# Kernel tuning notes

Hardware: AMD Instinct MI355X
Metric: run time of the kernel (lower is better)

Reference implementation:

```python
import jax, jax.numpy as jnp
import numpy as np

WINDOW = 512
N_GLOBAL = 32


def setup_inputs() -> dict:
    key = jax.random.key(0)
    kq, kk, kv = jax.random.split(key, 3)
    shape = (2, 16, 8192, 64)  # [batch, heads, seq_len, head_dim]
    q = jax.random.normal(kq, shape, dtype=jnp.float32)
    k = jax.random.normal(kk, shape, dtype=jnp.float32)
    v = jax.random.normal(kv, shape, dtype=jnp.float32)
    return {"q": q, "k": k, "v": v}


def _sliding_window_attention(q, k, v):
    # Faithful to the torch loop: for i in range(0, S, W) the window is
    # [max(0, i-W//2), min(S, i+W//2)). For S a multiple of W these windows are
    # contiguous, non-overlapping chunks: chunk0 = [0, W//2), then (n-1) chunks
    # of width W. Concatenated output covers positions [0, S - W//2).
    B, H, S, D = q.shape
    W, G, half = WINDOW, N_GLOBAL, WINDOW // 2
    n = S // W
    scale = 1.0 / (D ** 0.5)

    kg = k[:, :, :G]  # [B,H,G,D] global keys
    vg = v[:, :, :G]

    # --- first chunk: positions [0, half) ---
    q0 = q[:, :, :half]
    kc0 = jnp.concatenate([kg, k[:, :, :half]], axis=2)  # [B,H,G+half,D]
    vc0 = jnp.concatenate([vg, v[:, :, :half]], axis=2)
    s0 = jnp.einsum('bhqd,bhkd->bhqk', q0, kc0) * scale
    o0 = jnp.einsum('bhqk,bhkd->bhqd', jax.nn.softmax(s0, axis=-1), vc0)

    # --- remaining (n-1) chunks of width W: positions [half, S-half) ---
    C = n - 1
    qr = q[:, :, half:S - half].reshape(B, H, C, W, D)
    kr = k[:, :, half:S - half].reshape(B, H, C, W, D)
    vr = v[:, :, half:S - half].reshape(B, H, C, W, D)
    kgb = jnp.broadcast_to(kg[:, :, None], (B, H, C, G, D))
    vgb = jnp.broadcast_to(vg[:, :, None], (B, H, C, G, D))
    kc = jnp.concatenate([kgb, kr], axis=3)  # [B,H,C,G+W,D]
    vc = jnp.concatenate([vgb, vr], axis=3)
    s = jnp.einsum('bhcqd,bhckd->bhcqk', qr, kc) * scale
    o = jnp.einsum('bhcqk,bhckd->bhcqd', jax.nn.softmax(s, axis=-1), vc)
    o = o.reshape(B, H, C * W, D)

    return jnp.concatenate([o0, o], axis=2)  # [B,H,S - W//2,D]


def reference(q, k, v):
    return _sliding_window_attention(q, k, v)
```

## Files before the change

kernel.cpp:

```cpp
#include <hip/hip_runtime.h>
#include <hip/hip_bf16.h>

typedef __bf16 v8bf16 __attribute__((ext_vector_type(8)));
typedef __bf16 v2bf16 __attribute__((ext_vector_type(2)));
typedef float  v4f    __attribute__((ext_vector_type(4)));
typedef float  v16f   __attribute__((ext_vector_type(16)));
typedef unsigned int u32;

#define SEQ     8192
#define DIM     64
#define OUTSEQ  7936
#define WIN     512
#define HALF    256
#define BH      32
#define NCHUNK  15
#define MAXT    17
#define NWG_CH  1920
#define VROWT   40

__device__ __forceinline__ v8bf16 cvt8(v4f a, v4f b) {
    v8bf16 r;
    r[0] = (__bf16)a[0]; r[1] = (__bf16)a[1];
    r[2] = (__bf16)a[2]; r[3] = (__bf16)a[3];
    r[4] = (__bf16)b[0]; r[5] = (__bf16)b[1];
    r[6] = (__bf16)b[2]; r[7] = (__bf16)b[3];
    return r;
}

__device__ __forceinline__ v8bf16 load8bf(const float* __restrict__ p) {
    const v4f a = *(const v4f*)p;
    const v4f b = *(const v4f*)(p + 4);
    return cvt8(a, b);
}

__device__ __forceinline__ u32 pk2(float lo, float hi) {
    v2bf16 p; p[0] = (__bf16)lo; p[1] = (__bf16)hi;
    return __builtin_bit_cast(u32, p);
}

__device__ __forceinline__ int vt_idx(int d, int col) {
    return d * VROWT + (col ^ (((d >> 3) & 3) << 3));
}

__global__ __launch_bounds__(256, 4)
void swa_fwd(const float* __restrict__ qg,
             const float* __restrict__ kg,
             const float* __restrict__ vg,
             float* __restrict__ outg)
{
    __shared__ __align__(16) __bf16 Vt[2][DIM * VROWT];

    const int b = blockIdx.x;
    int bh, qoff, koff, ntiles;
    if (b < NWG_CH) {
        const int x  = b & 7;
        const int j  = b >> 3;
        const int qt = j & 3;
        const int cg = ((j >> 2) << 3) | x;
        bh = cg / NCHUNK;
        const int c = cg - bh * NCHUNK;
        koff = HALF + c * WIN;
        qoff = koff + qt * 128;
        ntiles = MAXT;
    } else {
        const int i = b - NWG_CH;
        bh = i >> 1;
        qoff = (i & 1) * 128;
        koff = 0;
        ntiles = 9;
    }

    const float* qb = qg + (size_t)bh * SEQ * DIM;
    const float* kb = kg + (size_t)bh * SEQ * DIM;
    const float* vb = vg + (size_t)bh * SEQ * DIM;

    const int tid  = threadIdx.x;
    const int wave = tid >> 6;
    const int lane = tid & 63;
    const int l31  = lane & 31;
    const int hi8  = (lane >> 5) * 8;

    const int qrow = qoff + wave * 32 + l31;
    v8bf16 qf[4];
    {
        const float* qp = qb + (size_t)qrow * DIM + hi8;
        #pragma unroll
        for (int c = 0; c < 4; ++c) qf[c] = load8bf(qp + c * 16);
    }

    const int keyduo = tid >> 4;
    const int dquad  = tid & 15;

    {
        const int tokA = 2 * keyduo;
        const v4f a  = *(const v4f*)(vb + (size_t)tokA * DIM + dquad * 4);
        const v4f b2 = *(const v4f*)(vb + (size_t)(tokA + 1) * DIM + dquad * 4);
        #pragma unroll
        for (int i = 0; i < 4; ++i) {
            v2bf16 pr; pr[0] = (__bf16)a[i]; pr[1] = (__bf16)b2[i];
            *(v2bf16*)(&Vt[0][vt_idx(dquad * 4 + i, 2 * keyduo)]) = pr;
        }
    }
    __syncthreads();

    const float cexp = 0.125f * 1.44269504089f;
    const v16f z16 = {0.f,0.f,0.f,0.f,0.f,0.f,0.f,0.f,
                      0.f,0.f,0.f,0.f,0.f,0.f,0.f,0.f};
    float lsum = 0.f;
    v16f oacc[2];
    oacc[0] = z16; oacc[1] = z16;

    int cur = 0;
    for (int t = 0; t < ntiles; ++t) {
        const int base = (t == 0) ? 0 : koff + (t - 1) * 32;
        const bool have_next = (t + 1 < ntiles);

        v4f sva, svb;
        if (have_next) {
            const int tokA = koff + t * 32 + 2 * keyduo;
            sva = *(const v4f*)(vb + (size_t)tokA * DIM + dquad * 4);
            svb = *(const v4f*)(vb + (size_t)(tokA + 1) * DIM + dquad * 4);
        }

        v8bf16 kf[4];
        {
            const float* kp = kb + (size_t)(base + l31) * DIM + hi8;
            #pragma unroll
            for (int c = 0; c < 4; ++c) kf[c] = load8bf(kp + c * 16);
        }

        const __bf16* vcur = Vt[cur];
        v8bf16 vf[2][2];
        #pragma unroll
        for (int dt = 0; dt < 2; ++dt)
            #pragma unroll
            for (int ks = 0; ks < 2; ++ks)
                vf[dt][ks] = *(const v8bf16*)(&vcur[vt_idx(dt * 32 + l31, ks * 16 + hi8)]);

        v16f s = __builtin_amdgcn_mfma_f32_32x32x16_bf16(kf[0], qf[0], z16, 0,0,0);
        s = __builtin_amdgcn_mfma_f32_32x32x16_bf16(kf[1], qf[1], s, 0,0,0);
        s = __builtin_amdgcn_mfma_f32_32x32x16_bf16(kf[2], qf[2], s, 0,0,0);
        s = __builtin_amdgcn_mfma_f32_32x32x16_bf16(kf[3], qf[3], s, 0,0,0);

        u32 P[8];
        float lacc = 0.f;
        #pragma unroll
        for (int r = 0; r < 16; r += 2) {
            const float ea = __builtin_exp2f(s[r]     * cexp);
            const float eb = __builtin_exp2f(s[r + 1] * cexp);
            lacc += ea + eb;
            P[r >> 1] = pk2(ea, eb);
        }
        lsum += lacc;

        asm volatile("v_permlane32_swap_b32 %0, %1" : "+v"(P[0]), "+v"(P[2]));
        asm volatile("v_permlane32_swap_b32 %0, %1" : "+v"(P[1]), "+v"(P[3]));
        asm volatile("v_permlane32_swap_b32 %0, %1" : "+v"(P[4]), "+v"(P[6]));
        asm volatile("v_permlane32_swap_b32 %0, %1" : "+v"(P[5]), "+v"(P[7]));

        const v8bf16 pf0 = __builtin_bit_cast(v8bf16, *(const u32(*)[4])&P[0]);
        const v8bf16 pf1 = __builtin_bit_cast(v8bf16, *(const u32(*)[4])&P[4]);

        oacc[0] = __builtin_amdgcn_mfma_f32_32x32x16_bf16(vf[0][0], pf0, oacc[0], 0,0,0);
        oacc[1] = __builtin_amdgcn_mfma_f32_32x32x16_bf16(vf[1][0], pf0, oacc[1], 0,0,0);
        oacc[0] = __builtin_amdgcn_mfma_f32_32x32x16_bf16(vf[0][1], pf1, oacc[0], 0,0,0);
        oacc[1] = __builtin_amdgcn_mfma_f32_32x32x16_bf16(vf[1][1], pf1, oacc[1], 0,0,0);

        if (have_next) {
            __bf16* vnxt = Vt[cur ^ 1];
            #pragma unroll
            for (int i = 0; i < 4; ++i) {
                v2bf16 pr; pr[0] = (__bf16)sva[i]; pr[1] = (__bf16)svb[i];
                *(v2bf16*)(&vnxt[vt_idx(dquad * 4 + i, 2 * keyduo)]) = pr;
            }
        }
        __syncthreads();
        cur ^= 1;
    }

    const float l = lsum + __shfl_xor(lsum, 32, 64);
    const float inv = 1.0f / l;
    float* ob = outg + ((size_t)bh * OUTSEQ + qrow) * DIM + (lane >> 5) * 4;
    #pragma unroll
    for (int dt = 0; dt < 2; ++dt) {
        #pragma unroll
        for (int rg = 0; rg < 4; ++rg) {
            v4f rv;
            rv[0] = oacc[dt][rg * 4 + 0] * inv;
            rv[1] = oacc[dt][rg * 4 + 1] * inv;
            rv[2] = oacc[dt][rg * 4 + 2] * inv;
            rv[3] = oacc[dt][rg * 4 + 3] * inv;
            *(v4f*)(ob + dt * 32 + rg * 8) = rv;
        }
    }
}

extern "C" void kernel_launch(void* const* d_in, const int* in_sizes, int n_in,
                              void* d_out, int out_size, void* d_ws, size_t ws_size,
                              hipStream_t stream) {
    const float* q = (const float*)d_in[0];
    const float* k = (const float*)d_in[1];
    const float* v = (const float*)d_in[2];
    float* out = (float*)d_out;

    const int n_wg = NWG_CH + BH * 2;
    swa_fwd<<<dim3(n_wg), dim3(256), 0, stream>>>(q, k, v, out);
}
```

Before: 293.9 us.

## Load V fragments directly from global memory, dropping LDS transpose and barriers

Removes the double-buffered shared-memory transpose of V and the per-tile __syncthreads. Each wave now builds its MFMA V operands by gathering strided scalar fp32 loads straight from global memory and packing them to bf16. This drops LDS traffic and block-wide synchronisation. The cost is that each wave loads the V tile on its own, so there are four times more global loads, and they are uncoalesced scalar accesses that lean heavily on the cache.

```diff
diff --git a/kernel.cpp b/kernel.cpp
--- a/kernel.cpp
+++ b/kernel.cpp
@@ -16,7 +16,6 @@
 #define NCHUNK  15
 #define MAXT    17
 #define NWG_CH  1920
-#define VROWT   40
 
 __device__ __forceinline__ v8bf16 cvt8(v4f a, v4f b) {
     v8bf16 r;
@@ -38,18 +37,12 @@
     return __builtin_bit_cast(u32, p);
 }
 
-__device__ __forceinline__ int vt_idx(int d, int col) {
-    return d * VROWT + (col ^ (((d >> 3) & 3) << 3));
-}
-
 __global__ __launch_bounds__(256, 4)
 void swa_fwd(const float* __restrict__ qg,
              const float* __restrict__ kg,
              const float* __restrict__ vg,
              float* __restrict__ outg)
 {
-    __shared__ __align__(16) __bf16 Vt[2][DIM * VROWT];
-
     const int b = blockIdx.x;
     int bh, qoff, koff, ntiles;
     if (b < NWG_CH) {
@@ -88,21 +81,6 @@
         for (int c = 0; c < 4; ++c) qf[c] = load8bf(qp + c * 16);
     }
 
-    const int keyduo = tid >> 4;
-    const int dquad  = tid & 15;
-
-    {
-        const int tokA = 2 * keyduo;
-        const v4f a  = *(const v4f*)(vb + (size_t)tokA * DIM + dquad * 4);
-        const v4f b2 = *(const v4f*)(vb + (size_t)(tokA + 1) * DIM + dquad * 4);
-        #pragma unroll
-        for (int i = 0; i < 4; ++i) {
-            v2bf16 pr; pr[0] = (__bf16)a[i]; pr[1] = (__bf16)b2[i];
-            *(v2bf16*)(&Vt[0][vt_idx(dquad * 4 + i, 2 * keyduo)]) = pr;
-        }
-    }
-    __syncthreads();
-
     const float cexp = 0.125f * 1.44269504089f;
     const v16f z16 = {0.f,0.f,0.f,0.f,0.f,0.f,0.f,0.f,
                       0.f,0.f,0.f,0.f,0.f,0.f,0.f,0.f};
@@ -110,16 +88,23 @@
     v16f oacc[2];
     oacc[0] = z16; oacc[1] = z16;
 
-    int cur = 0;
     for (int t = 0; t < ntiles; ++t) {
         const int base = (t == 0) ? 0 : koff + (t - 1) * 32;
-        const bool have_next = (t + 1 < ntiles);
 
-        v4f sva, svb;
-        if (have_next) {
-            const int tokA = koff + t * 32 + 2 * keyduo;
-            sva = *(const v4f*)(vb + (size_t)tokA * DIM + dquad * 4);
-            svb = *(const v4f*)(vb + (size_t)(tokA + 1) * DIM + dquad * 4);
+        v8bf16 vf[2][2];
+        #pragma unroll
+        for (int dt = 0; dt < 2; ++dt) {
+            #pragma unroll
+            for (int ks = 0; ks < 2; ++ks) {
+                const float* vp = vb + (size_t)(base + ks * 16 + hi8) * DIM + dt * 32 + l31;
+                float f[8];
+                #pragma unroll
+                for (int j = 0; j < 8; ++j) f[j] = vp[j * DIM];
+                u32 w[4];
+                #pragma unroll
+                for (int p = 0; p < 4; ++p) w[p] = pk2(f[2 * p], f[2 * p + 1]);
+                vf[dt][ks] = __builtin_bit_cast(v8bf16, w);
+            }
         }
 
         v8bf16 kf[4];
@@ -128,14 +113,6 @@
             #pragma unroll
             for (int c = 0; c < 4; ++c) kf[c] = load8bf(kp + c * 16);
         }
-
-        const __bf16* vcur = Vt[cur];
-        v8bf16 vf[2][2];
-        #pragma unroll
-        for (int dt = 0; dt < 2; ++dt)
-            #pragma unroll
-            for (int ks = 0; ks < 2; ++ks)
-                vf[dt][ks] = *(const v8bf16*)(&vcur[vt_idx(dt * 32 + l31, ks * 16 + hi8)]);
 
         v16f s = __builtin_amdgcn_mfma_f32_32x32x16_bf16(kf[0], qf[0], z16, 0,0,0);
         s = __builtin_amdgcn_mfma_f32_32x32x16_bf16(kf[1], qf[1], s, 0,0,0);
@@ -165,17 +142,6 @@
         oacc[1] = __builtin_amdgcn_mfma_f32_32x32x16_bf16(vf[1][0], pf0, oacc[1], 0,0,0);
         oacc[0] = __builtin_amdgcn_mfma_f32_32x32x16_bf16(vf[0][1], pf1, oacc[0], 0,0,0);
         oacc[1] = __builtin_amdgcn_mfma_f32_32x32x16_bf16(vf[1][1], pf1, oacc[1], 0,0,0);
-
-        if (have_next) {
-            __bf16* vnxt = Vt[cur ^ 1];
-            #pragma unroll
-            for (int i = 0; i < 4; ++i) {
-                v2bf16 pr; pr[0] = (__bf16)sva[i]; pr[1] = (__bf16)svb[i];
-                *(v2bf16*)(&vnxt[vt_idx(dquad * 4 + i, 2 * keyduo)]) = pr;
-            }
-        }
-        __syncthreads();
-        cur ^= 1;
     }
 
     const float l = lsum + __shfl_xor(lsum, 32, 64);
```

After: 332.6 us. 13.2% more time.
